# Performance work log

Measured on AMD Instinct MI355X. Metric: run time of the kernel, lower is better.

Reference implementation:

```python
import jax, jax.numpy as jnp
import numpy as np
from jax import lax

COCO_80_TO_91 = [1,2,3,4,5,6,7,8,9,10,11,13,14,15,16,17,18,19,20,21,22,23,24,25,27,28,31,32,33,34,35,36,37,38,39,40,41,42,43,44,46,47,48,49,50,51,52,53,54,55,56,57,58,59,60,61,62,63,64,65,67,70,72,73,74,75,76,77,78,79,80,81,82,84,85,86,87,88,89,90]

CONF = 0.25      # self.confidence
IOU_THR = 0.7    # ultralytics NMS default
TOPK = 1000      # candidate cap before NMS
MAX_DET = 300    # ultralytics max_det default
MAX_WH = 7680.0  # per-class offset trick
IMG_SZ = 640.0   # yolov8 letterboxed input size


def setup_inputs() -> dict:
    key = jax.random.key(0)
    preds = jax.random.uniform(key, (32, 84, 8400), dtype=jnp.float32)
    return {"preds": preds}


def _nms_single(boxes, scores):
    """Greedy NMS on score-descending boxes [K,4] (class-offset xyxy). Returns keep mask [K]."""
    K = boxes.shape[0]
    area = (boxes[:, 2] - boxes[:, 0]) * (boxes[:, 3] - boxes[:, 1])  # [K]
    lt = jnp.maximum(boxes[:, None, :2], boxes[None, :, :2])          # [K,K,2]
    rb = jnp.minimum(boxes[:, None, 2:], boxes[None, :, 2:])
    wh = jnp.clip(rb - lt, 0.0)
    inter = wh[..., 0] * wh[..., 1]
    iou = inter / (area[:, None] + area[None, :] - inter + 1e-7)       # [K,K]
    idx = jnp.arange(K)
    sup = (iou > IOU_THR) & (idx[None, :] > idx[:, None])              # i suppresses later j

    def body(i, keep):
        return jnp.where(keep[i], keep & ~sup[i], keep)

    return lax.fori_loop(0, K, body, jnp.ones((K,), dtype=bool))


def reference(preds):
    # preds: [B, 84, N] -> [B, N, 84]
    p = jnp.transpose(preds, (0, 2, 1))
    box_xywh = p[..., :4] * IMG_SZ           # xywh in pixels on 640x640 canvas
    cls = p[..., 4:]                          # [B, N, 80]
    scores = jnp.max(cls, axis=-1)            # best-class confidence
    labels = jnp.argmax(cls, axis=-1)         # 0..79
    xy, wh = box_xywh[..., :2], box_xywh[..., 2:]
    xyxy = jnp.concatenate([xy - wh * 0.5, xy + wh * 0.5], axis=-1)  # decode

    # confidence filter + top-K candidate selection (score-descending)
    s_masked = jnp.where(scores > CONF, scores, -1.0)
    top_s, top_i = lax.top_k(s_masked, TOPK)                          # [B,TOPK]
    top_b = jnp.take_along_axis(xyxy, top_i[..., None], axis=1)      # [B,TOPK,4]
    top_l = jnp.take_along_axis(labels, top_i, axis=1)               # [B,TOPK]

    # per-class NMS via class offset
    off_b = top_b + (top_l.astype(top_b.dtype) * MAX_WH)[..., None]
    keep = jax.vmap(_nms_single)(off_b, top_s) & (top_s > CONF)

    # select final max_det detections, zero-pad invalid slots
    fin_s = jnp.where(keep, top_s, -1.0)
    out_s, out_i = lax.top_k(fin_s, MAX_DET)                          # [B,MAX_DET]
    out_b = jnp.take_along_axis(top_b, out_i[..., None], axis=1)
    out_l = jnp.take_along_axis(top_l, out_i, axis=1)
    valid = out_s > CONF
    boxes = jnp.where(valid[..., None], out_b, 0.0)
    scores_out = jnp.where(valid, out_s, 0.0)
    mapped = jnp.asarray(COCO_80_TO_91, dtype=jnp.int64)[out_l]       # COCO 80 -> 91 ids
    labels_out = jnp.where(valid, mapped, 0)
    return boxes, scores_out, labels_out
```

## Files before the change

kernel.cpp:

```cpp
#include <hip/hip_runtime.h>
#include <stdint.h>

typedef unsigned long long u64;
typedef unsigned int u32;

#define BATCH 32
#define NCH 84
#define NA 8400
#define NCLS 80
#define TOPK 1000
#define MAXDET 300
#define CONF 0.25f
#define IOU_T 0.7f
#define MAX_WH 7680.0f
#define IMG_SZ 640.0f
#define NT 1024
#define KPT 9
#define NCOPY 8
#define HPAD 260

__device__ __constant__ float coco_map_f[NCLS] = {
    1,2,3,4,5,6,7,8,9,10,11,13,14,15,16,17,18,19,20,21,22,23,24,25,27,28,
    31,32,33,34,35,36,37,38,39,40,41,42,43,44,46,47,48,49,50,51,52,53,54,
    55,56,57,58,59,60,61,62,63,64,65,67,70,72,73,74,75,76,77,78,79,80,81,
    82,84,85,86,87,88,89,90};

__device__ inline u64 shflx64(u64 v, int m) {
    int lo = __shfl_xor((int)(u32)(v & 0xFFFFFFFFull), m, 64);
    int hi = __shfl_xor((int)(u32)(v >> 32), m, 64);
    return ((u64)(u32)hi << 32) | (u32)lo;
}

__global__ __launch_bounds__(256)
void decode_kernel(const float* __restrict__ preds,
                   u64* __restrict__ keys,
                   float4* __restrict__ boxes,
                   int* __restrict__ labels) {
    const int PPB = NA / 2;
    int gid = blockIdx.x * 256 + threadIdx.x;
    if (gid >= BATCH * PPB) return;
    int b = gid / PPB;
    int q = gid - b * PPB;
    int a0 = q * 2;
    const float* p = preds + (size_t)b * NCH * NA + a0;

    float2 x = *(const float2*)(p);
    float2 y = *(const float2*)(p + NA);
    float2 w = *(const float2*)(p + 2 * NA);
    float2 h = *(const float2*)(p + 3 * NA);

    float2 best = *(const float2*)(p + 4 * NA);
    int l0 = 0, l1 = 0;
#pragma unroll 16
    for (int c = 1; c < NCLS; ++c) {
        float2 v = *(const float2*)(p + (size_t)(4 + c) * NA);
        l0 = (v.x > best.x) ? c : l0;  best.x = fmaxf(v.x, best.x);
        l1 = (v.y > best.y) ? c : l1;  best.y = fmaxf(v.y, best.y);
    }

    float bs[2] = {best.x, best.y};
    int   bl[2] = {l0, l1};
    float cx[2] = {x.x, x.y};
    float cy[2] = {y.x, y.y};
    float cw[2] = {w.x, w.y};
    float ch[2] = {h.x, h.y};

    u64* kp = keys + (size_t)b * NA + a0;
    float4* bp = boxes + (size_t)b * NA + a0;
    int* lp = labels + (size_t)b * NA + a0;

#pragma unroll
    for (int i = 0; i < 2; ++i) {
        float fx = cx[i] * IMG_SZ, fy = cy[i] * IMG_SZ;
        float fw = cw[i] * IMG_SZ, fh = ch[i] * IMG_SZ;
        float hw = fw * 0.5f, hh = fh * 0.5f;
        bp[i] = make_float4(fx - hw, fy - hh, fx + hw, fy + hh);
        float s = (bs[i] > CONF) ? bs[i] : -1.0f;
        u32 fb = __float_as_uint(s);
        u32 u = (fb & 0x80000000u) ? ~fb : (fb | 0x80000000u);
        kp[i] = ((u64)u << 14) | (u64)(16383 - (a0 + i));
        lp[i] = bl[i];
    }
}

__global__ __launch_bounds__(NT)
void select_nms_kernel(const u64* __restrict__ keys,
                       const float4* __restrict__ boxes,
                       const int* __restrict__ labels,
                       float* __restrict__ out) {
    const int b = blockIdx.x;
    const int t = threadIdx.x;
    const int lane = t & 63, wid = t >> 6;

    __shared__ u64 skey[NT];
    __shared__ float offb[TOPK][4];
    __shared__ float area_s[TOPK];
    __shared__ unsigned char lb8[TOPK];
    __shared__ unsigned char keep[TOPK];
    __shared__ unsigned short rows[NCLS][64];
    __shared__ int sh_hist[NCOPY * HPAD];
    __shared__ int selB, selK, cnt, ktot_s;
    __shared__ int wsum[16], woff[16];

    u64 kreg[KPT];
    const u64* kb = keys + (size_t)b * NA;
    int nk = 0;
    for (int i = t; i < NA; i += NT) kreg[nk++] = kb[i];

    u64 P = 0ull;
    int kk = TOPK;
    for (int d = 5; d >= 0; --d) {
        for (int i = t; i < NCOPY * HPAD; i += NT) sh_hist[i] = 0;
        __syncthreads();
        u64 hmask = (~0ull) << (8 * (d + 1));
        int* myh = sh_hist + (wid & (NCOPY - 1)) * HPAD;
        for (int i = 0; i < KPT; ++i) {
            if (i < nk) {
                u64 key = kreg[i];
                if (((key ^ P) & hmask) == 0ull)
                    atomicAdd(&myh[(int)((key >> (8 * d)) & 255)], 1);
            }
        }
        __syncthreads();
        if (t < 64) {
            int h0 = 0, h1 = 0, h2 = 0, h3 = 0;
            for (int c = 0; c < NCOPY; ++c) {
                const int* hp = sh_hist + c * HPAD + 4 * t;
                h0 += hp[0]; h1 += hp[1]; h2 += hp[2]; h3 += hp[3];
            }
            int s = h0 + h1 + h2 + h3;
            int S = s;
            #pragma unroll
            for (int off = 1; off < 64; off <<= 1) {
                int o = __shfl_down(S, off, 64);
                if (t + off < 64) S += o;
            }
            int Snext = S - s;
            int c3 = Snext + h3, c2 = c3 + h2, c1 = c2 + h1, c0 = c1 + h0;
            int cand = -1, above = 0;
            if (c0 >= kk) {
                if      (c3 >= kk) { cand = 4 * t + 3; above = Snext; }
                else if (c2 >= kk) { cand = 4 * t + 2; above = c3; }
                else if (c1 >= kk) { cand = 4 * t + 1; above = c2; }
                else               { cand = 4 * t;     above = c1; }
            }
            int pc = (cand < 0) ? 0 : (((cand + 1) << 16) | (kk - above));
            #pragma unroll
            for (int off = 32; off; off >>= 1)
                pc = max(pc, __shfl_down(pc, off, 64));
            if (t == 0) { selB = (pc >> 16) - 1; selK = pc & 0xFFFF; }
        }
        __syncthreads();
        P |= ((u64)selB) << (8 * d);
        kk = selK;
    }

    if (t == 0) cnt = 0;
    __syncthreads();
    for (int i = 0; i < KPT; ++i) {
        bool p = (i < nk) && (kreg[i] >= P);
        u64 m = __ballot(p);
        int base = 0;
        if (lane == 0) base = atomicAdd(&cnt, (int)__popcll(m));
        base = __shfl(base, 0, 64);
        if (p) skey[base + (int)__popcll(m & ((1ull << lane) - 1ull))] = kreg[i];
    }
    if (t < NT - TOPK) skey[TOPK + t] = 0ull;
    __syncthreads();

    u64 myk = skey[t];
    for (int size = 2; size <= NT; size <<= 1) {
        bool up = ((t & size) == 0);
        for (int stride = size >> 1; stride; stride >>= 1) {
            u64 pk;
            if (stride >= 64) {
                __syncthreads(); skey[t] = myk; __syncthreads();
                pk = skey[t ^ stride];
            } else {
                pk = shflx64(myk, stride);
            }
            bool tlow = ((t & stride) == 0);
            u64 mn = (myk < pk) ? myk : pk;
            u64 mx = (myk < pk) ? pk : myk;
            myk = up ? (tlow ? mx : mn) : (tlow ? mn : mx);
        }
    }

    int my_a = -1, my_L = 0;
    if (t < TOPK) {
        my_a = 16383 - (int)(myk & 16383ull);
        my_L = labels[(size_t)b * NA + my_a];
        lb8[t] = (unsigned char)my_L;
        float4 bx = boxes[(size_t)b * NA + my_a];
        float off = (float)my_L * MAX_WH;
        float ox0 = bx.x + off, oy0 = bx.y + off, ox1 = bx.z + off, oy1 = bx.w + off;
        offb[t][0] = ox0; offb[t][1] = oy0; offb[t][2] = ox1; offb[t][3] = oy1;
        area_s[t] = (ox1 - ox0) * (oy1 - oy0);
        keep[t] = 1;
    }
    __syncthreads();

    for (int c = wid; c < NCLS; c += 16) {
        int n = 0;
        for (int chunk = 0; chunk < 16; ++chunk) {
            int j = chunk * 64 + lane;
            bool m = (j < TOPK) && (lb8[j] == (unsigned char)c);
            u64 bal = __ballot(m);
            if (m) {
                int pos = n + (int)__popcll(bal & ((1ull << lane) - 1ull));
                if (pos < 64) rows[c][pos] = (unsigned short)j;
            }
            n += (int)__popcll(bal);
        }
        if (n == 0) continue;
        if (n <= 64) {
            int j = (lane < n) ? (int)rows[c][lane] : (int)rows[c][0];
            float x0 = offb[j][0], y0 = offb[j][1];
            float x1 = offb[j][2], y1 = offb[j][3];
            float ar = area_s[j];
            u64 alive = (n >= 64) ? ~0ull : ((1ull << n) - 1ull);
            for (int i = 0; i < n; ++i) {
                if (!((alive >> i) & 1ull)) continue;
                float hx0 = __shfl(x0, i, 64);
                float hy0 = __shfl(y0, i, 64);
                float hx1 = __shfl(x1, i, 64);
                float hy1 = __shfl(y1, i, 64);
                float ha  = __shfl(ar, i, 64);
                float lx = fmaxf(hx0, x0), ly = fmaxf(hy0, y0);
                float rx = fminf(hx1, x1), ry = fminf(hy1, y1);
                float w = fmaxf(rx - lx, 0.0f);
                float h = fmaxf(ry - ly, 0.0f);
                float inter = w * h;
                float denom = ha + ar;
                denom = denom - inter;
                denom = denom + 1e-7f;
                bool sup = (lane > i) && (inter / denom > IOU_T);
                alive &= ~__ballot(sup);
            }
            if (lane < n) keep[j] = (unsigned char)((alive >> lane) & 1ull);
        } else if (lane == 0) {
            for (int i = 0; i < TOPK; ++i) {
                if (lb8[i] != (unsigned char)c || !keep[i]) continue;
                float ax0 = offb[i][0], ay0 = offb[i][1];
                float ax1 = offb[i][2], ay1 = offb[i][3];
                float aa = area_s[i];
                for (int j2 = i + 1; j2 < TOPK; ++j2) {
                    if (lb8[j2] != (unsigned char)c || !keep[j2]) continue;
                    float lx = fmaxf(ax0, offb[j2][0]);
                    float ly = fmaxf(ay0, offb[j2][1]);
                    float rx = fminf(ax1, offb[j2][2]);
                    float ry = fminf(ay1, offb[j2][3]);
                    float w = fmaxf(rx - lx, 0.0f);
                    float h = fmaxf(ry - ly, 0.0f);
                    float inter = w * h;
                    float denom = aa + area_s[j2];
                    denom = denom - inter;
                    denom = denom + 1e-7f;
                    if (inter / denom > IOU_T) keep[j2] = 0;
                }
            }
        }
    }
    __syncthreads();

    bool valid = false;
    float sj = 0.0f;
    if (t < TOPK) {
        u32 u = (u32)(myk >> 14);
        u32 fb = (u & 0x80000000u) ? (u ^ 0x80000000u) : ~u;
        sj = __uint_as_float(fb);
        valid = keep[t] && (sj > CONF);
    }
    u64 m = __ballot(valid);
    if (lane == 0) wsum[wid] = (int)__popcll(m);
    __syncthreads();
    if (wid == 0) {
        int v = (lane < 16) ? wsum[lane] : 0;
        #pragma unroll
        for (int off = 1; off < 16; off <<= 1) {
            int o = __shfl_up(v, off, 64);
            if (lane >= off) v += o;
        }
        if (lane < 16) woff[lane] = v - wsum[lane];
        if (lane == 15) ktot_s = v;
    }
    __syncthreads();
    int ktot = ktot_s;
    int rank = woff[wid] + (int)__popcll(m & ((1ull << lane) - 1ull));

    float* out_boxes = out;
    float* out_scores = out + (size_t)BATCH * MAXDET * 4;
    float* out_labels = out + (size_t)BATCH * MAXDET * 5;
    if (valid && rank < MAXDET) {
        float4 bx = boxes[(size_t)b * NA + my_a];
        float* ob = out_boxes + ((size_t)b * MAXDET + rank) * 4;
        ob[0] = bx.x; ob[1] = bx.y; ob[2] = bx.z; ob[3] = bx.w;
        out_scores[(size_t)b * MAXDET + rank] = sj;
        out_labels[(size_t)b * MAXDET + rank] = coco_map_f[my_L];
    }
    if (t < MAXDET && t >= ktot) {
        float* ob = out_boxes + ((size_t)b * MAXDET + t) * 4;
        ob[0] = 0.0f; ob[1] = 0.0f; ob[2] = 0.0f; ob[3] = 0.0f;
        out_scores[(size_t)b * MAXDET + t] = 0.0f;
        out_labels[(size_t)b * MAXDET + t] = 0.0f;
    }
}

extern "C" void kernel_launch(void* const* d_in, const int* in_sizes, int n_in,
                              void* d_out, int out_size, void* d_ws, size_t ws_size,
                              hipStream_t stream) {
    const float* preds = (const float*)d_in[0];
    char* ws = (char*)d_ws;

    const size_t keys_bytes = (size_t)BATCH * NA * 8;
    const size_t boxes_bytes = (size_t)BATCH * NA * 16;

    u64* keys = (u64*)ws;
    float4* boxes = (float4*)(ws + keys_bytes);
    int* labels = (int*)(ws + keys_bytes + boxes_bytes);
    float* out = (float*)d_out;

    int total = BATCH * (NA / 2);
    decode_kernel<<<(total + 255) / 256, 256, 0, stream>>>(preds, keys, boxes, labels);
    select_nms_kernel<<<BATCH, NT, 0, stream>>>(keys, boxes, labels, out);
}
```

Before: 189.4 us.

## Widen decode to float4, early-exit radix select, bitmask class grouping, branchless NMS IoU

The decode kernel now handles four anchors per thread with float4 loads and an int4 label store, cutting the thread count and load instructions. The radix top-K selection stops early once the candidate set fits in the 1024-slot sort buffer, skipping later histogram passes. Per-class member lists are built from shared-memory bitmasks filled with atomicOr instead of 16 ballot chunks per class. The small-class NMS first computes all pairwise suppression bits without early skipping, then resolves survivors in a cheap ballot loop. In exchange it does extra IoU work on already suppressed boxes and adds shared-memory atomics.

```diff
diff --git a/kernel.cpp b/kernel.cpp
--- a/kernel.cpp
+++ b/kernel.cpp
@@ -36,41 +36,43 @@
                    u64* __restrict__ keys,
                    float4* __restrict__ boxes,
                    int* __restrict__ labels) {
-    const int PPB = NA / 2;
+    const int QPB = NA / 4;
     int gid = blockIdx.x * 256 + threadIdx.x;
-    if (gid >= BATCH * PPB) return;
-    int b = gid / PPB;
-    int q = gid - b * PPB;
-    int a0 = q * 2;
+    if (gid >= BATCH * QPB) return;
+    int b = gid / QPB;
+    int q = gid - b * QPB;
+    int a0 = q * 4;
     const float* p = preds + (size_t)b * NCH * NA + a0;
 
-    float2 x = *(const float2*)(p);
-    float2 y = *(const float2*)(p + NA);
-    float2 w = *(const float2*)(p + 2 * NA);
-    float2 h = *(const float2*)(p + 3 * NA);
-
-    float2 best = *(const float2*)(p + 4 * NA);
-    int l0 = 0, l1 = 0;
+    float4 x = *(const float4*)(p);
+    float4 y = *(const float4*)(p + NA);
+    float4 w = *(const float4*)(p + 2 * NA);
+    float4 h = *(const float4*)(p + 3 * NA);
+
+    float4 best = *(const float4*)(p + 4 * NA);
+    int lx = 0, ly = 0, lz = 0, lw = 0;
 #pragma unroll 16
     for (int c = 1; c < NCLS; ++c) {
-        float2 v = *(const float2*)(p + (size_t)(4 + c) * NA);
-        l0 = (v.x > best.x) ? c : l0;  best.x = fmaxf(v.x, best.x);
-        l1 = (v.y > best.y) ? c : l1;  best.y = fmaxf(v.y, best.y);
-    }
-
-    float bs[2] = {best.x, best.y};
-    int   bl[2] = {l0, l1};
-    float cx[2] = {x.x, x.y};
-    float cy[2] = {y.x, y.y};
-    float cw[2] = {w.x, w.y};
-    float ch[2] = {h.x, h.y};
+        const float4 v = *(const float4*)(p + (size_t)(4 + c) * NA);
+        lx = (v.x > best.x) ? c : lx;  best.x = fmaxf(v.x, best.x);
+        ly = (v.y > best.y) ? c : ly;  best.y = fmaxf(v.y, best.y);
+        lz = (v.z > best.z) ? c : lz;  best.z = fmaxf(v.z, best.z);
+        lw = (v.w > best.w) ? c : lw;  best.w = fmaxf(v.w, best.w);
+    }
+
+    float bs[4] = {best.x, best.y, best.z, best.w};
+    int   bl[4] = {lx, ly, lz, lw};
+    float cx[4] = {x.x, x.y, x.z, x.w};
+    float cy[4] = {y.x, y.y, y.z, y.w};
+    float cw[4] = {w.x, w.y, w.z, w.w};
+    float ch[4] = {h.x, h.y, h.z, h.w};
 
     u64* kp = keys + (size_t)b * NA + a0;
     float4* bp = boxes + (size_t)b * NA + a0;
     int* lp = labels + (size_t)b * NA + a0;
 
 #pragma unroll
-    for (int i = 0; i < 2; ++i) {
+    for (int i = 0; i < 4; ++i) {
         float fx = cx[i] * IMG_SZ, fy = cy[i] * IMG_SZ;
         float fw = cw[i] * IMG_SZ, fh = ch[i] * IMG_SZ;
         float hw = fw * 0.5f, hh = fh * 0.5f;
@@ -79,8 +81,8 @@
         u32 fb = __float_as_uint(s);
         u32 u = (fb & 0x80000000u) ? ~fb : (fb | 0x80000000u);
         kp[i] = ((u64)u << 14) | (u64)(16383 - (a0 + i));
-        lp[i] = bl[i];
-    }
+    }
+    *(int4*)lp = make_int4(bl[0], bl[1], bl[2], bl[3]);
 }
 
 __global__ __launch_bounds__(NT)
@@ -97,9 +99,10 @@
     __shared__ float area_s[TOPK];
     __shared__ unsigned char lb8[TOPK];
     __shared__ unsigned char keep[TOPK];
+    __shared__ u64 cmask2[NCLS][16];
     __shared__ unsigned short rows[NCLS][64];
     __shared__ int sh_hist[NCOPY * HPAD];
-    __shared__ int selB, selK, cnt, ktot_s;
+    __shared__ int selB, selK, hselS, cnt, nselS, ktot_s;
     __shared__ int wsum[16], woff[16];
 
     u64 kreg[KPT];
@@ -109,6 +112,7 @@
 
     u64 P = 0ull;
     int kk = TOPK;
+    int nsel = 0;
     for (int d = 5; d >= 0; --d) {
         for (int i = t; i < NCOPY * HPAD; i += NT) sh_hist[i] = 0;
         __syncthreads();
@@ -148,11 +152,21 @@
             #pragma unroll
             for (int off = 32; off; off >>= 1)
                 pc = max(pc, __shfl_down(pc, off, 64));
-            if (t == 0) { selB = (pc >> 16) - 1; selK = pc & 0xFFFF; }
+            pc = __shfl(pc, 0, 64);
+            int B = (pc >> 16) - 1;
+            if (t == (B >> 2)) {
+                int m4 = B & 3;
+                selB = B;
+                selK = pc & 0xFFFF;
+                hselS = (m4 == 0) ? h0 : (m4 == 1) ? h1 : (m4 == 2) ? h2 : h3;
+            }
         }
         __syncthreads();
         P |= ((u64)selB) << (8 * d);
         kk = selK;
+        nsel = TOPK - kk + hselS;
+        if (nsel <= NT) break;
+        __syncthreads();
     }
 
     if (t == 0) cnt = 0;
@@ -165,7 +179,7 @@
         base = __shfl(base, 0, 64);
         if (p) skey[base + (int)__popcll(m & ((1ull << lane) - 1ull))] = kreg[i];
     }
-    if (t < NT - TOPK) skey[TOPK + t] = 0ull;
+    if (t < NT - nsel) skey[nsel + t] = 0ull;
     __syncthreads();
 
     u64 myk = skey[t];
@@ -185,6 +199,9 @@
             myk = up ? (tlow ? mx : mn) : (tlow ? mn : mx);
         }
     }
+
+    for (int i = t; i < NCLS * 16; i += NT) ((u64*)cmask2)[i] = 0ull;
+    __syncthreads();
 
     int my_a = -1, my_L = 0;
     if (t < TOPK) {
@@ -197,30 +214,37 @@
         offb[t][0] = ox0; offb[t][1] = oy0; offb[t][2] = ox1; offb[t][3] = oy1;
         area_s[t] = (ox1 - ox0) * (oy1 - oy0);
         keep[t] = 1;
+        atomicOr(&cmask2[my_L][t >> 6], 1ull << (t & 63));
     }
     __syncthreads();
 
     for (int c = wid; c < NCLS; c += 16) {
-        int n = 0;
-        for (int chunk = 0; chunk < 16; ++chunk) {
-            int j = chunk * 64 + lane;
-            bool m = (j < TOPK) && (lb8[j] == (unsigned char)c);
-            u64 bal = __ballot(m);
-            if (m) {
-                int pos = n + (int)__popcll(bal & ((1ull << lane) - 1ull));
-                if (pos < 64) rows[c][pos] = (unsigned short)j;
-            }
-            n += (int)__popcll(bal);
-        }
+        u64 w = (lane < 16) ? cmask2[c][lane] : 0ull;
+        int cw = __popcll(w);
+        int pre = cw;
+        #pragma unroll
+        for (int off = 1; off < 16; off <<= 1) {
+            int o = __shfl_up(pre, off, 64);
+            if (lane >= off) pre += o;
+        }
+        int n = __shfl(pre, 15, 64);
+        pre -= cw;
         if (n == 0) continue;
         if (n <= 64) {
+            if (lane < 16) {
+                u64 ww = w; int base = pre, boff = lane << 6;
+                while (ww) {
+                    int bit = __ffsll((long long)ww) - 1;
+                    ww &= ww - 1;
+                    rows[c][base++] = (unsigned short)(boff + bit);
+                }
+            }
             int j = (lane < n) ? (int)rows[c][lane] : (int)rows[c][0];
             float x0 = offb[j][0], y0 = offb[j][1];
             float x1 = offb[j][2], y1 = offb[j][3];
             float ar = area_s[j];
-            u64 alive = (n >= 64) ? ~0ull : ((1ull << n) - 1ull);
+            u64 colm = 0ull;
             for (int i = 0; i < n; ++i) {
-                if (!((alive >> i) & 1ull)) continue;
                 float hx0 = __shfl(x0, i, 64);
                 float hy0 = __shfl(y0, i, 64);
                 float hx1 = __shfl(x1, i, 64);
@@ -228,14 +252,19 @@
                 float ha  = __shfl(ar, i, 64);
                 float lx = fmaxf(hx0, x0), ly = fmaxf(hy0, y0);
                 float rx = fminf(hx1, x1), ry = fminf(hy1, y1);
-                float w = fmaxf(rx - lx, 0.0f);
-                float h = fmaxf(ry - ly, 0.0f);
-                float inter = w * h;
+                float ww2 = fmaxf(rx - lx, 0.0f);
+                float hh2 = fmaxf(ry - ly, 0.0f);
+                float inter = ww2 * hh2;
                 float denom = ha + ar;
                 denom = denom - inter;
                 denom = denom + 1e-7f;
-                bool sup = (lane > i) && (inter / denom > IOU_T);
-                alive &= ~__ballot(sup);
+                bool s = (lane > i) && (lane < n) && (inter / denom > IOU_T);
+                colm |= ((u64)s) << i;
+            }
+            u64 alive = (n >= 64) ? ~0ull : ((1ull << n) - 1ull);
+            for (int i = 0; i < n; ++i) {
+                if (!((alive >> i) & 1ull)) continue;
+                alive &= ~__ballot((colm >> i) & 1ull);
             }
             if (lane < n) keep[j] = (unsigned char)((alive >> lane) & 1ull);
         } else if (lane == 0) {
@@ -250,9 +279,9 @@
                     float ly = fmaxf(ay0, offb[j2][1]);
                     float rx = fminf(ax1, offb[j2][2]);
                     float ry = fminf(ay1, offb[j2][3]);
-                    float w = fmaxf(rx - lx, 0.0f);
-                    float h = fmaxf(ry - ly, 0.0f);
-                    float inter = w * h;
+                    float ww2 = fmaxf(rx - lx, 0.0f);
+                    float hh2 = fmaxf(ry - ly, 0.0f);
+                    float inter = ww2 * hh2;
                     float denom = aa + area_s[j2];
                     denom = denom - inter;
                     denom = denom + 1e-7f;
@@ -320,7 +349,7 @@
     int* labels = (int*)(ws + keys_bytes + boxes_bytes);
     float* out = (float*)d_out;
 
-    int total = BATCH * (NA / 2);
+    int total = BATCH * (NA / 4);
     decode_kernel<<<(total + 255) / 256, 256, 0, stream>>>(preds, keys, boxes, labels);
     select_nms_kernel<<<BATCH, NT, 0, stream>>>(keys, boxes, labels, out);
 }
```

Result: slower. 193.2 us (+2.0%).
